# Performance work log

Measured on AMD Instinct MI355X. Metric: run time of the kernel, lower is better.

The kernel has to match this reference:

```python
import jax, jax.numpy as jnp
import numpy as np

B, L, D = 4, 2048, 1024

def setup_inputs() -> dict:
    key = jax.random.key(0)
    k = jax.random.split(key, 5)
    s = 1.0 / np.sqrt(D)
    return {
        "x": jax.random.normal(k[0], (B, L, D), dtype=jnp.float32),
        "W1": jax.random.uniform(k[1], (D, D), jnp.float32, -s, s),
        "b1": jax.random.uniform(k[2], (D,), jnp.float32, -s, s),
        "W2": jax.random.uniform(k[3], (D, D), jnp.float32, -s, s),
        "b2": jax.random.uniform(k[4], (D,), jnp.float32, -s, s),
    }

def reference(x, W1, b1, W2, b2):
    # query = fc1(x), value = fc2(x); torch Linear: x @ W^T + b
    query = jnp.einsum("bld,ed->ble", x, W1) + b1   # [B,L,D]
    value = jnp.einsum("bld,ed->ble", x, W2) + b2   # [B,L,D]
    # attn = softmax(query @ value^T)  (dot attention, no scaling in original)
    scores = jnp.einsum("bqd,bkd->bqk", query, value)  # [B,L,L]
    attn = jax.nn.softmax(scores, axis=-1)
    # dropout_p=0.0 -> identity
    return jnp.einsum("bqk,bkd->bqd", attn, value)     # [B,L,D]
```

## Files before the change

kernel.cpp:

```cpp
#include <hip/hip_runtime.h>
#include <stdint.h>
#include <stddef.h>


typedef _Float16  f16_t;
typedef _Float16  f16x8 __attribute__((ext_vector_type(8)));
typedef float     f32x4 __attribute__((ext_vector_type(4)));

__device__ __forceinline__ f32x4 mfma16(f16x8 a, f16x8 b, f32x4 c) {
  return __builtin_amdgcn_mfma_f32_16x16x32_f16(a, b, c, 0, 0, 0);
}

__device__ __forceinline__ void async_copy16(const f16_t* g, f16_t* l) {
  __builtin_amdgcn_global_load_lds(
      (const __attribute__((address_space(1))) unsigned int*)(g),
      (__attribute__((address_space(3))) unsigned int*)(l),
      16, 0, 0);
}

template <int RM, int RN, int NS>
__device__ __forceinline__ void gemm_core(
    const f16_t* __restrict__ A, const f16_t* __restrict__ B,
    int lda, int ldb, int nk,
    f16_t* __restrict__ As, f16_t* __restrict__ Bs, f32x4 (&acc)[RM][RN])
{
  const int tid  = threadIdx.x;
  const int lane = tid & 63;
  const int w    = tid >> 6;
  const int wr   = (w >> 1) * (RM * 16);
  const int wc   = (w & 1) * (RN * 16);
  const int l16  = lane & 15;
  const int quad = lane >> 4;
  const int sw   = (quad ^ ((l16 >> 1) & 3)) * 8;

  const int r0  = tid >> 2;
  const int kc0 = ((tid & 3) ^ ((r0 >> 1) & 3)) * 8;

  const f16_t* Ag = A + (size_t)r0 * lda + kc0;
  const f16_t* Bg = B + (size_t)r0 * ldb + kc0;

  for (int kt = 0; kt < nk; ++kt) {
#pragma unroll
    for (int s = 0; s < NS; ++s) {
      const int ko = s * 32;
#pragma unroll
      for (int h = 0; h < RM / 2; ++h)
        async_copy16(Ag + ko + (size_t)(64 * h) * lda,
                     As + s * RM * 1024 + (tid + 256 * h) * 8);
#pragma unroll
      for (int h = 0; h < RN / 2; ++h)
        async_copy16(Bg + ko + (size_t)(64 * h) * ldb,
                     Bs + s * RN * 1024 + (tid + 256 * h) * 8);
    }
    __syncthreads();

#pragma unroll
    for (int s = 0; s < NS; ++s) {
      const f16_t* Ac = As + s * RM * 1024;
      const f16_t* Bc = Bs + s * RN * 1024;
      f16x8 af[RM], bf[RN];
#pragma unroll
      for (int i = 0; i < RM; ++i)
        af[i] = *(const f16x8*)(Ac + (wr + i * 16 + l16) * 32 + sw);
#pragma unroll
      for (int j = 0; j < RN; ++j)
        bf[j] = *(const f16x8*)(Bc + (wc + j * 16 + l16) * 32 + sw);
#pragma unroll
      for (int i = 0; i < RM; ++i)
#pragma unroll
        for (int j = 0; j < RN; ++j)
          acc[i][j] = mfma16(af[i], bf[j], acc[i][j]);
    }

    __syncthreads();
    Ag += NS * 32; Bg += NS * 32;
  }
}

__global__ __launch_bounds__(256) void cvt_kernel(
    const float* __restrict__ x, const float* __restrict__ W1,
    const float* __restrict__ W2, f16_t* __restrict__ xh,
    f16_t* __restrict__ W1h, f16_t* __restrict__ W2h)
{
  const size_t XN = (size_t)8192 * 1024;
  const size_t WN = (size_t)1024 * 1024;
  size_t i = ((size_t)blockIdx.x * 256 + threadIdx.x) * 8;
  const float* in; f16_t* out;
  if (i < XN)            { in = x;  out = xh; }
  else if (i < XN + WN)  { in = W1; out = W1h; i -= XN; }
  else                   { in = W2; out = W2h; i -= XN + WN; }
  f32x4 a = *(const f32x4*)(in + i);
  f32x4 b = *(const f32x4*)(in + i + 4);
  f16x8 o;
#pragma unroll
  for (int k = 0; k < 4; ++k) { o[k] = (f16_t)a[k]; o[k + 4] = (f16_t)b[k]; }
  *(f16x8*)(out + i) = o;
}

__global__ __launch_bounds__(256) void proj_qv_kernel(
    const f16_t* __restrict__ X, const f16_t* __restrict__ W1,
    const f16_t* __restrict__ W2, const float* __restrict__ b1,
    const float* __restrict__ b2, f16_t* __restrict__ Q,
    f16_t* __restrict__ V, f16_t* __restrict__ Vt)
{
  __shared__ __align__(16) f16_t smem[16384];
  f16_t* Xs  = smem;
  f16_t* W1s = smem + 8192;
  f16_t* W2s = smem + 12288;
  constexpr int XSZ = 128 * 32;
  constexpr int WSZ = 64 * 32;

  const int m0 = blockIdx.x * 128;
  const int n0 = blockIdx.y * 64;

  const int tid  = threadIdx.x;
  const int lane = tid & 63;
  const int w    = tid >> 6;
  const int wr   = (w >> 1) * 64;
  const int wc   = (w & 1) * 32;
  const int quad = lane >> 4;
  const int l16  = lane & 15;
  const int sw   = (quad ^ ((l16 >> 1) & 3)) * 8;
  const int r0   = tid >> 2;
  const int kc0  = ((tid & 3) ^ ((r0 >> 1) & 3)) * 8;

  const f16_t* Xg = X + (size_t)(m0 + r0) * 1024 + kc0;
  const f16_t* G1 = W1 + (size_t)(n0 + r0) * 1024 + kc0;
  const f16_t* G2 = W2 + (size_t)(n0 + r0) * 1024 + kc0;

  f32x4 accQ[4][2] = {};
  f32x4 accV[4][2] = {};

  for (int kt = 0; kt < 16; ++kt) {
#pragma unroll
    for (int s = 0; s < 2; ++s) {
      const int ko = s * 32;
      async_copy16(Xg + ko, Xs + s * XSZ + tid * 8);
      async_copy16(Xg + ko + (size_t)64 * 1024, Xs + s * XSZ + (tid + 256) * 8);
      async_copy16(G1 + ko, W1s + s * WSZ + tid * 8);
      async_copy16(G2 + ko, W2s + s * WSZ + tid * 8);
    }
    __syncthreads();

#pragma unroll
    for (int s = 0; s < 2; ++s) {
      f16x8 xf[4], w1f[2], w2f[2];
#pragma unroll
      for (int i = 0; i < 4; ++i)
        xf[i]  = *(const f16x8*)(Xs  + s * XSZ + (wr + i * 16 + l16) * 32 + sw);
#pragma unroll
      for (int j = 0; j < 2; ++j) {
        w1f[j] = *(const f16x8*)(W1s + s * WSZ + (wc + j * 16 + l16) * 32 + sw);
        w2f[j] = *(const f16x8*)(W2s + s * WSZ + (wc + j * 16 + l16) * 32 + sw);
      }
#pragma unroll
      for (int i = 0; i < 4; ++i)
#pragma unroll
        for (int j = 0; j < 2; ++j) {
          accQ[i][j] = mfma16(xf[i], w1f[j], accQ[i][j]);
          accV[i][j] = mfma16(xf[i], w2f[j], accV[i][j]);
        }
    }
    __syncthreads();
    Xg += 64; G1 += 64; G2 += 64;
  }

  f16_t* Ts = smem;
#pragma unroll
  for (int j = 0; j < 2; ++j) {
    const int c   = wc + j * 16 + l16;
    const int col = n0 + c;
    const float bq = b1[col], bv = b2[col];
#pragma unroll
    for (int i = 0; i < 4; ++i)
#pragma unroll
      for (int r = 0; r < 4; ++r) {
        const int k   = wr + i * 16 + quad * 4 + r;
        const int row = m0 + k;
        const float q = accQ[i][j][r] + bq;
        const float v = accV[i][j][r] + bv;
        Q[(size_t)row * 1024 + col] = (f16_t)q;
        V[(size_t)row * 1024 + col] = (f16_t)v;
        Ts[c * 136 + k] = (f16_t)v;
      }
  }
  __syncthreads();

  const size_t vtbase = ((size_t)(m0 >> 11) << 21) + (size_t)n0 * 2048 + (m0 & 2047);
#pragma unroll
  for (int rep = 0; rep < 4; ++rep) {
    const int d  = rep * 16 + (tid >> 4);
    const int c4 = tid & 15;
    f16x8 vv = *(const f16x8*)(Ts + d * 136 + c4 * 8);
    *(f16x8*)(Vt + vtbase + (size_t)d * 2048 + c4 * 8) = vv;
  }
}

__global__ __launch_bounds__(256) void score_kernel(
    const f16_t* __restrict__ Q, const f16_t* __restrict__ V,
    f16_t* __restrict__ S)
{
  __shared__ __align__(16) f16_t As[2 * 128 * 32];
  __shared__ __align__(16) f16_t Bs[2 * 128 * 32];
  const int m0 = blockIdx.x * 128;
  const int n0 = blockIdx.y * 128;
  const size_t boff = (size_t)blockIdx.z * 2048 * 1024;

  f32x4 acc[4][4] = {};
  gemm_core<4, 4, 2>(Q + boff + (size_t)m0 * 1024,
                     V + boff + (size_t)n0 * 1024,
                     1024, 1024, 1024 / 64, As, Bs, acc);

  f16_t* Sb = S + (size_t)blockIdx.z * 2048 * 2048;
  const int lane = threadIdx.x & 63;
  const int w    = threadIdx.x >> 6;
  const int wr   = (w >> 1) * 64, wc = (w & 1) * 64;
  const int quad = lane >> 4,     l16 = lane & 15;

#pragma unroll
  for (int i = 0; i < 4; ++i)
#pragma unroll
    for (int j = 0; j < 4; ++j)
#pragma unroll
      for (int r = 0; r < 4; ++r) {
        const int row = m0 + wr + i * 16 + quad * 4 + r;
        const int col = n0 + wc + j * 16 + l16;
        Sb[(size_t)row * 2048 + col] = (f16_t)acc[i][j][r];
      }
}

__global__ __launch_bounds__(256) void softmax_kernel(f16_t* __restrict__ S)
{
  const int tid    = threadIdx.x;
  const int lane32 = tid & 31;
  const int rowid  = blockIdx.x * 8 + (tid >> 5);
  f16_t* row = S + (size_t)rowid * 2048;

  f16x8 v[8];
#pragma unroll
  for (int c = 0; c < 8; ++c)
    v[c] = *(const f16x8*)(row + c * 256 + lane32 * 8);

  float m = -3.0e38f;
#pragma unroll
  for (int c = 0; c < 8; ++c)
#pragma unroll
    for (int k = 0; k < 8; ++k) m = fmaxf(m, (float)v[c][k]);
#pragma unroll
  for (int off = 16; off >= 1; off >>= 1) m = fmaxf(m, __shfl_xor(m, off));

  float s = 0.f;
  float e[8][8];
#pragma unroll
  for (int c = 0; c < 8; ++c)
#pragma unroll
    for (int k = 0; k < 8; ++k) {
      e[c][k] = __expf((float)v[c][k] - m);
      s += e[c][k];
    }
#pragma unroll
  for (int off = 16; off >= 1; off >>= 1) s += __shfl_xor(s, off);
  const float inv = 1.f / s;

#pragma unroll
  for (int c = 0; c < 8; ++c) {
    f16x8 o;
#pragma unroll
    for (int k = 0; k < 8; ++k) o[k] = (f16_t)(e[c][k] * inv);
    *(f16x8*)(row + c * 256 + lane32 * 8) = o;
  }
}

__global__ __launch_bounds__(256) void out_kernel(
    const f16_t* __restrict__ P, const f16_t* __restrict__ Vt,
    float* __restrict__ Out)
{
  __shared__ __align__(16) f16_t As[2 * 128 * 32];
  __shared__ __align__(16) f16_t Bs[2 * 128 * 32];
  const int m0 = blockIdx.x * 128;
  const int n0 = blockIdx.y * 128;
  const size_t poff  = (size_t)blockIdx.z * 2048 * 2048;
  const size_t vtoff = (size_t)blockIdx.z * 1024 * 2048;

  f32x4 acc[4][4] = {};
  gemm_core<4, 4, 2>(P + poff + (size_t)m0 * 2048,
                     Vt + vtoff + (size_t)n0 * 2048,
                     2048, 2048, 2048 / 64, As, Bs, acc);

  float* Ob = Out + (size_t)blockIdx.z * 2048 * 1024;
  const int lane = threadIdx.x & 63;
  const int w    = threadIdx.x >> 6;
  const int wr   = (w >> 1) * 64, wc = (w & 1) * 64;
  const int quad = lane >> 4,     l16 = lane & 15;

#pragma unroll
  for (int i = 0; i < 4; ++i)
#pragma unroll
    for (int j = 0; j < 4; ++j)
#pragma unroll
      for (int r = 0; r < 4; ++r) {
        const int row = m0 + wr + i * 16 + quad * 4 + r;
        const int col = n0 + wc + j * 16 + l16;
        Ob[(size_t)row * 1024 + col] = acc[i][j][r];
      }
}

extern "C" void kernel_launch(void* const* d_in, const int* in_sizes, int n_in,
                              void* d_out, int out_size, void* d_ws, size_t ws_size,
                              hipStream_t stream) {
  const float* x  = (const float*)d_in[0];
  const float* W1 = (const float*)d_in[1];
  const float* b1 = (const float*)d_in[2];
  const float* W2 = (const float*)d_in[3];
  const float* b2 = (const float*)d_in[4];
  float* out = (float*)d_out;

  const size_t QN = (size_t)8192 * 1024;
  const size_t WN = (size_t)1024 * 1024;
  f16_t* xh  = (f16_t*)d_ws;
  f16_t* W1h = xh + QN;
  f16_t* W2h = W1h + WN;
  f16_t* Q   = W2h + WN;
  f16_t* V   = Q + QN;
  f16_t* Vt  = V + QN;
  f16_t* S   = Vt + QN;

  dim3 blk(256);
  cvt_kernel<<<5120, blk, 0, stream>>>(x, W1, W2, xh, W1h, W2h);
  proj_qv_kernel<<<dim3(64, 16), blk, 0, stream>>>(xh, W1h, W2h, b1, b2, Q, V, Vt);
  score_kernel<<<dim3(16, 16, 4), blk, 0, stream>>>(Q, V, S);
  softmax_kernel<<<1024, blk, 0, stream>>>(S);
  out_kernel<<<dim3(16, 8, 4), blk, 0, stream>>>(S, Vt, out);
}
```

Measured before the change: 225.6 us.

## Double-buffer LDS tiles so async global loads overlap MFMA compute

Replaces the load-all-then-compute loop, which staged two K-slices per iteration, with a ping-pong double buffer holding one 32-wide K slice per buffer. The next slice is prefetched via global_load_lds while MFMAs consume the current one, in both the shared GEMM core and the fused projection kernel. This removes one of the two barriers per step and aims to hide global-load latency behind compute. In exchange, each step now does half as much MFMA work per barrier, so barrier count per unit of work is unchanged. Correctness depends on the single barrier per step also ordering the async LDS writes, which may be fragile.

```diff
diff --git a/kernel.cpp b/kernel.cpp
--- a/kernel.cpp
+++ b/kernel.cpp
@@ -18,12 +18,15 @@
       16, 0, 0);
 }
 
-template <int RM, int RN, int NS>
+template <int RM, int RN>
 __device__ __forceinline__ void gemm_core(
     const f16_t* __restrict__ A, const f16_t* __restrict__ B,
     int lda, int ldb, int nk,
     f16_t* __restrict__ As, f16_t* __restrict__ Bs, f32x4 (&acc)[RM][RN])
 {
+  constexpr int ASZ = RM * 1024;
+  constexpr int BSZ = RN * 1024;
+
   const int tid  = threadIdx.x;
   const int lane = tid & 63;
   const int w    = tid >> 6;
@@ -39,41 +42,42 @@
   const f16_t* Ag = A + (size_t)r0 * lda + kc0;
   const f16_t* Bg = B + (size_t)r0 * ldb + kc0;
 
-  for (int kt = 0; kt < nk; ++kt) {
-#pragma unroll
-    for (int s = 0; s < NS; ++s) {
-      const int ko = s * 32;
-#pragma unroll
-      for (int h = 0; h < RM / 2; ++h)
-        async_copy16(Ag + ko + (size_t)(64 * h) * lda,
-                     As + s * RM * 1024 + (tid + 256 * h) * 8);
-#pragma unroll
-      for (int h = 0; h < RN / 2; ++h)
-        async_copy16(Bg + ko + (size_t)(64 * h) * ldb,
-                     Bs + s * RN * 1024 + (tid + 256 * h) * 8);
-    }
+  auto stage = [&](int t, int buf) {
+    const size_t ko = (size_t)t * 32;
+#pragma unroll
+    for (int h = 0; h < RM / 2; ++h)
+      async_copy16(Ag + ko + (size_t)(64 * h) * lda,
+                   As + buf * ASZ + (tid + 256 * h) * 8);
+#pragma unroll
+    for (int h = 0; h < RN / 2; ++h)
+      async_copy16(Bg + ko + (size_t)(64 * h) * ldb,
+                   Bs + buf * BSZ + (tid + 256 * h) * 8);
+  };
+
+  stage(0, 0);
+  __syncthreads();
+
+  int buf = 0;
+  for (int t = 0; t < nk; ++t) {
+    if (t + 1 < nk) stage(t + 1, buf ^ 1);
+
+    const f16_t* Ac = As + buf * ASZ;
+    const f16_t* Bc = Bs + buf * BSZ;
+    f16x8 af[RM], bf[RN];
+#pragma unroll
+    for (int i = 0; i < RM; ++i)
+      af[i] = *(const f16x8*)(Ac + (wr + i * 16 + l16) * 32 + sw);
+#pragma unroll
+    for (int j = 0; j < RN; ++j)
+      bf[j] = *(const f16x8*)(Bc + (wc + j * 16 + l16) * 32 + sw);
+#pragma unroll
+    for (int i = 0; i < RM; ++i)
+#pragma unroll
+      for (int j = 0; j < RN; ++j)
+        acc[i][j] = mfma16(af[i], bf[j], acc[i][j]);
+
     __syncthreads();
-
-#pragma unroll
-    for (int s = 0; s < NS; ++s) {
-      const f16_t* Ac = As + s * RM * 1024;
-      const f16_t* Bc = Bs + s * RN * 1024;
-      f16x8 af[RM], bf[RN];
-#pragma unroll
-      for (int i = 0; i < RM; ++i)
-        af[i] = *(const f16x8*)(Ac + (wr + i * 16 + l16) * 32 + sw);
-#pragma unroll
-      for (int j = 0; j < RN; ++j)
-        bf[j] = *(const f16x8*)(Bc + (wc + j * 16 + l16) * 32 + sw);
-#pragma unroll
-      for (int i = 0; i < RM; ++i)
-#pragma unroll
-        for (int j = 0; j < RN; ++j)
-          acc[i][j] = mfma16(af[i], bf[j], acc[i][j]);
-    }
-
-    __syncthreads();
-    Ag += NS * 32; Bg += NS * 32;
+    buf ^= 1;
   }
 }
 
@@ -131,38 +135,40 @@
   f32x4 accQ[4][2] = {};
   f32x4 accV[4][2] = {};
 
-  for (int kt = 0; kt < 16; ++kt) {
-#pragma unroll
-    for (int s = 0; s < 2; ++s) {
-      const int ko = s * 32;
-      async_copy16(Xg + ko, Xs + s * XSZ + tid * 8);
-      async_copy16(Xg + ko + (size_t)64 * 1024, Xs + s * XSZ + (tid + 256) * 8);
-      async_copy16(G1 + ko, W1s + s * WSZ + tid * 8);
-      async_copy16(G2 + ko, W2s + s * WSZ + tid * 8);
+  auto stage = [&](int t, int buf) {
+    const size_t ko = (size_t)t * 32;
+    async_copy16(Xg + ko, Xs + buf * XSZ + tid * 8);
+    async_copy16(Xg + ko + (size_t)64 * 1024, Xs + buf * XSZ + (tid + 256) * 8);
+    async_copy16(G1 + ko, W1s + buf * WSZ + tid * 8);
+    async_copy16(G2 + ko, W2s + buf * WSZ + tid * 8);
+  };
+
+  stage(0, 0);
+  __syncthreads();
+
+  int buf = 0;
+  for (int t = 0; t < 32; ++t) {
+    if (t + 1 < 32) stage(t + 1, buf ^ 1);
+
+    f16x8 xf[4], w1f[2], w2f[2];
+#pragma unroll
+    for (int i = 0; i < 4; ++i)
+      xf[i]  = *(const f16x8*)(Xs  + buf * XSZ + (wr + i * 16 + l16) * 32 + sw);
+#pragma unroll
+    for (int j = 0; j < 2; ++j) {
+      w1f[j] = *(const f16x8*)(W1s + buf * WSZ + (wc + j * 16 + l16) * 32 + sw);
+      w2f[j] = *(const f16x8*)(W2s + buf * WSZ + (wc + j * 16 + l16) * 32 + sw);
     }
+#pragma unroll
+    for (int i = 0; i < 4; ++i)
+#pragma unroll
+      for (int j = 0; j < 2; ++j) {
+        accQ[i][j] = mfma16(xf[i], w1f[j], accQ[i][j]);
+        accV[i][j] = mfma16(xf[i], w2f[j], accV[i][j]);
+      }
+
     __syncthreads();
-
-#pragma unroll
-    for (int s = 0; s < 2; ++s) {
-      f16x8 xf[4], w1f[2], w2f[2];
-#pragma unroll
-      for (int i = 0; i < 4; ++i)
-        xf[i]  = *(const f16x8*)(Xs  + s * XSZ + (wr + i * 16 + l16) * 32 + sw);
-#pragma unroll
-      for (int j = 0; j < 2; ++j) {
-        w1f[j] = *(const f16x8*)(W1s + s * WSZ + (wc + j * 16 + l16) * 32 + sw);
-        w2f[j] = *(const f16x8*)(W2s + s * WSZ + (wc + j * 16 + l16) * 32 + sw);
-      }
-#pragma unroll
-      for (int i = 0; i < 4; ++i)
-#pragma unroll
-        for (int j = 0; j < 2; ++j) {
-          accQ[i][j] = mfma16(xf[i], w1f[j], accQ[i][j]);
-          accV[i][j] = mfma16(xf[i], w2f[j], accV[i][j]);
-        }
-    }
-    __syncthreads();
-    Xg += 64; G1 += 64; G2 += 64;
+    buf ^= 1;
   }
 
   f16_t* Ts = smem;
@@ -207,9 +213,9 @@
   const size_t boff = (size_t)blockIdx.z * 2048 * 1024;
 
   f32x4 acc[4][4] = {};
-  gemm_core<4, 4, 2>(Q + boff + (size_t)m0 * 1024,
-                     V + boff + (size_t)n0 * 1024,
-                     1024, 1024, 1024 / 64, As, Bs, acc);
+  gemm_core<4, 4>(Q + boff + (size_t)m0 * 1024,
+                  V + boff + (size_t)n0 * 1024,
+                  1024, 1024, 1024 / 32, As, Bs, acc);
 
   f16_t* Sb = S + (size_t)blockIdx.z * 2048 * 2048;
   const int lane = threadIdx.x & 63;
@@ -283,9 +289,9 @@
   const size_t vtoff = (size_t)blockIdx.z * 1024 * 2048;
 
   f32x4 acc[4][4] = {};
-  gemm_core<4, 4, 2>(P + poff + (size_t)m0 * 2048,
-                     Vt + vtoff + (size_t)n0 * 2048,
-                     2048, 2048, 2048 / 64, As, Bs, acc);
+  gemm_core<4, 4>(P + poff + (size_t)m0 * 2048,
+                  Vt + vtoff + (size_t)n0 * 2048,
+                  2048, 2048, 2048 / 32, As, Bs, acc);
 
   float* Ob = Out + (size_t)blockIdx.z * 2048 * 1024;
   const int lane = threadIdx.x & 63;
```

After: 255.9 us. 1.13x slower.

## Rewrite score GEMM with 256x256 tiles, 8 waves and manual async pipeline

Applied to the files above, without the earlier changes.

The score kernel now uses 512-thread blocks computing 256x256 output tiles with per-wave 128x64 accumulators. It replaces the generic gemm_core with a hand-scheduled loop that interleaves async global-to-LDS copies for the next K-step between MFMA groups, using explicit vmcnt waits, raw barriers, sched_barrier and setprio. The goal is more reuse per LDS load and better overlap of memory with MFMA work. The cost is higher register pressure (128 accumulator floats per lane), 128KB of LDS, and only 256 blocks, which can leave the chip's CUs unevenly loaded.

```diff
diff --git a/kernel.cpp b/kernel.cpp
--- a/kernel.cpp
+++ b/kernel.cpp
@@ -17,6 +17,10 @@
       (__attribute__((address_space(3))) unsigned int*)(l),
       16, 0, 0);
 }
+
+#define SCHED0() __builtin_amdgcn_sched_barrier(0)
+#define VMCNT(N) asm volatile("s_waitcnt vmcnt(" #N ")" ::: "memory")
+#define RAWBAR() asm volatile("s_barrier" ::: "memory")
 
 template <int RM, int RN, int NS>
 __device__ __forceinline__ void gemm_core(
@@ -196,35 +200,134 @@
   }
 }
 
-__global__ __launch_bounds__(256) void score_kernel(
+__global__ __launch_bounds__(512) void score_kernel(
     const f16_t* __restrict__ Q, const f16_t* __restrict__ V,
     f16_t* __restrict__ S)
 {
-  __shared__ __align__(16) f16_t As[2 * 128 * 32];
-  __shared__ __align__(16) f16_t Bs[2 * 128 * 32];
-  const int m0 = blockIdx.x * 128;
-  const int n0 = blockIdx.y * 128;
+  __shared__ __align__(16) f16_t As[4 * 8192];
+  __shared__ __align__(16) f16_t Bs[4 * 8192];
+  const int m0 = blockIdx.x * 256;
+  const int n0 = blockIdx.y * 256;
   const size_t boff = (size_t)blockIdx.z * 2048 * 1024;
-
-  f32x4 acc[4][4] = {};
-  gemm_core<4, 4, 2>(Q + boff + (size_t)m0 * 1024,
-                     V + boff + (size_t)n0 * 1024,
-                     1024, 1024, 1024 / 64, As, Bs, acc);
+  const f16_t* Ag = Q + boff + (size_t)m0 * 1024;
+  const f16_t* Bg = V + boff + (size_t)n0 * 1024;
+
+  const int tid  = threadIdx.x;
+  const int lane = tid & 63;
+  const int w    = tid >> 6;
+  const int wm   = w >> 2;
+  const int wn   = w & 3;
+  const int l16  = lane & 15;
+  const int quad = lane >> 4;
+  const int sw   = (quad ^ ((l16 >> 1) & 3)) * 8;
+
+  f32x4 acc[8][4] = {};
+
+  auto stage = [&](const f16_t* G, f16_t* L, int t, int s) {
+#pragma unroll
+    for (int rho = 0; rho < 2; ++rho) {
+      const int slot = tid + 512 * rho;
+      const int row  = slot >> 2;
+      const int ch   = slot & 3;
+      async_copy16(G + (size_t)row * 1024 + t * 64 + s * 32
+                     + ((ch ^ ((row >> 1) & 3)) << 3),
+                   L + ((t & 1) * 2 + s) * 8192 + slot * 8);
+    }
+  };
+
+  stage(Ag, As, 0, 0); stage(Bg, Bs, 0, 0);
+  stage(Ag, As, 0, 1); stage(Bg, Bs, 0, 1);
+
+  for (int t = 0; t < 16; ++t) {
+    const int d = t & 1;
+    const f16_t* A0 = As + (d * 2 + 0) * 8192;
+    const f16_t* B0 = Bs + (d * 2 + 0) * 8192;
+    const f16_t* A1 = As + (d * 2 + 1) * 8192;
+    const f16_t* B1 = Bs + (d * 2 + 1) * 8192;
+    const bool last = (t == 15);
+
+    if (!last) stage(Ag, As, t + 1, 0);
+    SCHED0();
+    if (!last) { VMCNT(6); } else { VMCNT(4); }
+    SCHED0();
+    RAWBAR();
+    {
+      f16x8 bf[4], af[4];
+#pragma unroll
+      for (int j = 0; j < 4; ++j)
+        bf[j] = *(const f16x8*)(B0 + (wn * 64 + j * 16 + l16) * 32 + sw);
+#pragma unroll
+      for (int i = 0; i < 4; ++i)
+        af[i] = *(const f16x8*)(A0 + (wm * 128 + i * 16 + l16) * 32 + sw);
+      __builtin_amdgcn_s_setprio(1);
+#pragma unroll
+      for (int i = 0; i < 4; ++i)
+#pragma unroll
+        for (int j = 0; j < 4; ++j)
+          acc[i][j] = mfma16(af[i], bf[j], acc[i][j]);
+      __builtin_amdgcn_s_setprio(0);
+      SCHED0();
+
+      if (!last) stage(Bg, Bs, t + 1, 0);
+#pragma unroll
+      for (int i = 0; i < 4; ++i)
+        af[i] = *(const f16x8*)(A0 + (wm * 128 + (4 + i) * 16 + l16) * 32 + sw);
+      __builtin_amdgcn_s_setprio(1);
+#pragma unroll
+      for (int i = 0; i < 4; ++i)
+#pragma unroll
+        for (int j = 0; j < 4; ++j)
+          acc[4 + i][j] = mfma16(af[i], bf[j], acc[4 + i][j]);
+      __builtin_amdgcn_s_setprio(0);
+      SCHED0();
+    }
+
+    if (!last) stage(Ag, As, t + 1, 1);
+    SCHED0();
+    if (!last) { VMCNT(6); } else { VMCNT(0); }
+    SCHED0();
+    RAWBAR();
+    {
+      f16x8 bf[4], af[4];
+#pragma unroll
+      for (int j = 0; j < 4; ++j)
+        bf[j] = *(const f16x8*)(B1 + (wn * 64 + j * 16 + l16) * 32 + sw);
+#pragma unroll
+      for (int i = 0; i < 4; ++i)
+        af[i] = *(const f16x8*)(A1 + (wm * 128 + i * 16 + l16) * 32 + sw);
+      __builtin_amdgcn_s_setprio(1);
+#pragma unroll
+      for (int i = 0; i < 4; ++i)
+#pragma unroll
+        for (int j = 0; j < 4; ++j)
+          acc[i][j] = mfma16(af[i], bf[j], acc[i][j]);
+      __builtin_amdgcn_s_setprio(0);
+      SCHED0();
+
+      if (!last) stage(Bg, Bs, t + 1, 1);
+#pragma unroll
+      for (int i = 0; i < 4; ++i)
+        af[i] = *(const f16x8*)(A1 + (wm * 128 + (4 + i) * 16 + l16) * 32 + sw);
+      __builtin_amdgcn_s_setprio(1);
+#pragma unroll
+      for (int i = 0; i < 4; ++i)
+#pragma unroll
+        for (int j = 0; j < 4; ++j)
+          acc[4 + i][j] = mfma16(af[i], bf[j], acc[4 + i][j]);
+      __builtin_amdgcn_s_setprio(0);
+      SCHED0();
+    }
+  }
 
   f16_t* Sb = S + (size_t)blockIdx.z * 2048 * 2048;
-  const int lane = threadIdx.x & 63;
-  const int w    = threadIdx.x >> 6;
-  const int wr   = (w >> 1) * 64, wc = (w & 1) * 64;
-  const int quad = lane >> 4,     l16 = lane & 15;
-
-#pragma unroll
-  for (int i = 0; i < 4; ++i)
+#pragma unroll
+  for (int i = 0; i < 8; ++i)
 #pragma unroll
     for (int j = 0; j < 4; ++j)
 #pragma unroll
       for (int r = 0; r < 4; ++r) {
-        const int row = m0 + wr + i * 16 + quad * 4 + r;
-        const int col = n0 + wc + j * 16 + l16;
+        const int row = m0 + wm * 128 + i * 16 + quad * 4 + r;
+        const int col = n0 + wn * 64 + j * 16 + l16;
         Sb[(size_t)row * 2048 + col] = (f16_t)acc[i][j][r];
       }
 }
@@ -325,10 +428,9 @@
   f16_t* Vt  = V + QN;
   f16_t* S   = Vt + QN;
 
-  dim3 blk(256);
-  cvt_kernel<<<5120, blk, 0, stream>>>(x, W1, W2, xh, W1h, W2h);
-  proj_qv_kernel<<<dim3(64, 16), blk, 0, stream>>>(xh, W1h, W2h, b1, b2, Q, V, Vt);
-  score_kernel<<<dim3(16, 16, 4), blk, 0, stream>>>(Q, V, S);
-  softmax_kernel<<<1024, blk, 0, stream>>>(S);
-  out_kernel<<<dim3(16, 8, 4), blk, 0, stream>>>(S, Vt, out);
-}
+  cvt_kernel<<<5120, 256, 0, stream>>>(x, W1, W2, xh, W1h, W2h);
+  proj_qv_kernel<<<dim3(64, 16), 256, 0, stream>>>(xh, W1h, W2h, b1, b2, Q, V, Vt);
+  score_kernel<<<dim3(8, 8, 4), 512, 0, stream>>>(Q, V, S);
+  softmax_kernel<<<1024, 256, 0, stream>>>(S);
+  out_kernel<<<dim3(16, 8, 4), 256, 0, stream>>>(S, Vt, out);
+}
```

Measured after the change: 228.5 us. No clear change (+1.3%).
